# Kernel tuning notes

Hardware: AMD Instinct MI355X
Metric: run time of the kernel (lower is better)

The kernel has to match this reference:

```python
import jax, jax.numpy as jnp
import numpy as np

# TT config (matches init_kwargs)
NUM_TABLES = 4
P = (100, 100, 100)          # tt_p_shapes, prod = num_embeddings = 1e6
Q = (4, 4, 4)                # tt_q_shapes, prod = embedding_dim = 64
R = (1, 32, 32, 1)           # tt_ranks with boundary ranks
BAGS_PER_TABLE = 8192
POOL = 16                    # indices per bag


def setup_inputs() -> dict:
    key = jax.random.key(0)
    k1, k2, k3, k4 = jax.random.split(key, 4)
    nnz = NUM_TABLES * BAGS_PER_TABLE * POOL      # 524288
    B = NUM_TABLES * BAGS_PER_TABLE               # 32768 bags total
    indices = jax.random.randint(k1, (nnz,), 0, P[0] * P[1] * P[2], dtype=jnp.int64)
    offsets = (jnp.arange(B + 1, dtype=jnp.int64) * POOL)
    scale = 0.05  # small init, akin to approx-normal weight_dist
    tt_core_0 = jax.random.normal(k2, (NUM_TABLES, P[0], R[0] * Q[0] * R[1]), dtype=jnp.float32) * scale
    tt_core_1 = jax.random.normal(k3, (NUM_TABLES, P[1], R[1] * Q[1] * R[2]), dtype=jnp.float32) * scale
    tt_core_2 = jax.random.normal(k4, (NUM_TABLES, P[2], R[2] * Q[2] * R[3]), dtype=jnp.float32) * scale
    return {"indices": indices, "offsets": offsets,
            "tt_core_0": tt_core_0, "tt_core_1": tt_core_1, "tt_core_2": tt_core_2}


def reference(indices, offsets, tt_core_0, tt_core_1, tt_core_2):
    nnz = indices.shape[0]
    B = offsets.shape[0] - 1
    bags_per_table = B // NUM_TABLES

    # bag id for each nonzero (embedding-bag semantics), then table id per nonzero
    rowidx = jnp.searchsorted(offsets, jnp.arange(nnz, dtype=offsets.dtype), side='right') - 1
    tableidx = rowidx // bags_per_table

    # decompose flat row index into TT indices (C-order over p-shapes,
    # matching tt_matrix_to_full row layout)
    i0 = indices // (P[1] * P[2])
    i1 = (indices // P[2]) % P[1]
    i2 = indices % P[2]

    # gather per-lookup core slices
    c0 = tt_core_0[tableidx, i0].reshape(nnz, Q[0], R[1])          # r0 == 1
    c1 = tt_core_1[tableidx, i1].reshape(nnz, R[1], Q[1], R[2])
    c2 = tt_core_2[tableidx, i2].reshape(nnz, R[2], Q[2])          # r3 == 1

    # on-the-fly TT contraction to reconstruct embedding rows [nnz, D]
    t = jnp.einsum('nar,nrbs->nabs', c0, c1)                       # [nnz, q0, q1, r2]
    rows = jnp.einsum('nabs,nsc->nabc', t, c2).reshape(nnz, Q[0] * Q[1] * Q[2])

    # sum-pool per bag
    out = jax.ops.segment_sum(rows, rowidx, num_segments=B)        # [B, D]
    return out
```

## Files before the change

### kernel.cpp

```cpp
#include <hip/hip_runtime.h>
#include <stdint.h>

#define NT 4
#define PP 100


__device__ __forceinline__ uint32_t f2bf(float f) {
    union { float f; uint32_t u; } v; v.f = f;
    uint32_t u = v.u;
    return (u + 0x7fffu + ((u >> 16) & 1u)) >> 16;
}

__global__ __launch_bounds__(128, 3)
void tt_phase1(const float* __restrict__ c0g, const float* __restrict__ c1g,
               unsigned short* __restrict__ tT) {
    __shared__ float c1s[32 * 128];
    __shared__ float c0t[16 * 132];

    int blk = blockIdx.x;
    int tab   = blk / 700;
    int rem   = blk % 700;
    int i1    = rem / 7;
    int chunk = rem % 7;
    int i0_base = chunk * 16;
    int tid = threadIdx.x;

    const float4* c1p = (const float4*)(c1g + (size_t)(tab * PP + i1) * 4096);
    float4* c1v = (float4*)c1s;
    #pragma unroll
    for (int it = 0; it < 8; ++it) c1v[tid + 128 * it] = c1p[tid + 128 * it];

    #pragma unroll
    for (int it = 0; it < 16; ++it) {
        int f = tid + 128 * it;
        int i0l = f >> 7;
        int x   = f & 127;
        int a = x >> 5, r = x & 31;
        int i0 = i0_base + i0l; if (i0 > PP - 1) i0 = PP - 1;
        c0t[i0l * 132 + r * 4 + a] = c0g[(size_t)(tab * PP + i0) * 128 + x];
    }
    __syncthreads();

    int u  = tid >> 4;
    int sg = tid & 15;

    float acc[2][2][16];
    #pragma unroll
    for (int ii = 0; ii < 2; ++ii)
        #pragma unroll
        for (int e = 0; e < 2; ++e)
            #pragma unroll
            for (int q = 0; q < 16; ++q) acc[ii][e][q] = 0.f;

    #pragma unroll 4
    for (int r = 0; r < 32; ++r) {
        float4 av0 = *(const float4*)&c0t[(2 * u) * 132 + r * 4];
        float4 av1 = *(const float4*)&c0t[(2 * u + 1) * 132 + r * 4];
        const float* a0 = (const float*)&av0;
        const float* a1 = (const float*)&av1;
        #pragma unroll
        for (int b = 0; b < 4; ++b) {
            float2 bv = *(const float2*)&c1s[r * 128 + b * 32 + 2 * sg];
            #pragma unroll
            for (int a = 0; a < 4; ++a) {
                acc[0][0][a * 4 + b] += a0[a] * bv.x;
                acc[0][1][a * 4 + b] += a0[a] * bv.y;
                acc[1][0][a * 4 + b] += a1[a] * bv.x;
                acc[1][1][a * 4 + b] += a1[a] * bv.y;
            }
        }
    }

    #pragma unroll
    for (int ii = 0; ii < 2; ++ii) {
        int i0 = i0_base + 2 * u + ii;
        if (i0 >= PP) continue;
        size_t combo = (size_t)tab * 10000 + (size_t)i0 * 100 + (size_t)i1;
        char* base = (char*)tT + combo * 1024 + (size_t)sg * 64;
        #pragma unroll
        for (int e = 0; e < 2; ++e) {
            uint4 w0, w1;
            w0.x = f2bf(acc[ii][e][0])  | (f2bf(acc[ii][e][1])  << 16);
            w0.y = f2bf(acc[ii][e][2])  | (f2bf(acc[ii][e][3])  << 16);
            w0.z = f2bf(acc[ii][e][4])  | (f2bf(acc[ii][e][5])  << 16);
            w0.w = f2bf(acc[ii][e][6])  | (f2bf(acc[ii][e][7])  << 16);
            w1.x = f2bf(acc[ii][e][8])  | (f2bf(acc[ii][e][9])  << 16);
            w1.y = f2bf(acc[ii][e][10]) | (f2bf(acc[ii][e][11]) << 16);
            w1.z = f2bf(acc[ii][e][12]) | (f2bf(acc[ii][e][13]) << 16);
            w1.w = f2bf(acc[ii][e][14]) | (f2bf(acc[ii][e][15]) << 16);
            *(uint4*)(base + e * 32)      = w0;
            *(uint4*)(base + e * 32 + 16) = w1;
        }
    }
}

__global__ __launch_bounds__(256, 2)
void tt_phase2(const int* __restrict__ indices, const int* __restrict__ offsets,
               const unsigned short* __restrict__ tT, const float* __restrict__ c2g,
               float* __restrict__ out, int bags_per_table, int B) {
    int lane = threadIdx.x & 63;
    int wv   = threadIdx.x >> 6;
    int bag  = blockIdx.x * 4 + wv;
    if (bag >= B) return;
    int sub = lane >> 4;
    int sg  = lane & 15;
    int tab = bag / bags_per_table;
    int start = offsets[bag];

    const float* c2t = c2g + (size_t)tab * PP * 128;

    const uint4*  tp[4];
    const float4* cp[4];
    #pragma unroll
    for (int j = 0; j < 4; ++j) {
        uint32_t idx = (uint32_t)indices[start + j * 4 + sub];
        uint32_t i0 = idx / 10000u;
        uint32_t r1 = idx - i0 * 10000u;
        uint32_t i1 = r1 / 100u;
        uint32_t i2 = r1 - i1 * 100u;
        tp[j] = (const uint4*)((const char*)tT +
                 ((size_t)tab * 10000u + i0 * 100u + i1) * 1024 + (size_t)sg * 64);
        cp[j] = (const float4*)(c2t + (size_t)i2 * 128 + sg * 8);
    }

    uint4  T[4][4];
    float4 C[4][2];
    #pragma unroll
    for (int j = 0; j < 4; ++j) {
        T[j][0] = tp[j][0]; T[j][1] = tp[j][1];
        T[j][2] = tp[j][2]; T[j][3] = tp[j][3];
        C[j][0] = cp[j][0]; C[j][1] = cp[j][1];
    }

    float acc[64];
    #pragma unroll
    for (int d = 0; d < 64; ++d) acc[d] = 0.f;

    #pragma unroll
    for (int j = 0; j < 4; ++j) {
        #pragma unroll
        for (int e = 0; e < 2; ++e) {
            float4 cv = C[j][e];
            uint32_t us[8] = { T[j][2*e].x, T[j][2*e].y, T[j][2*e].z, T[j][2*e].w,
                               T[j][2*e+1].x, T[j][2*e+1].y, T[j][2*e+1].z, T[j][2*e+1].w };
            #pragma unroll
            for (int k = 0; k < 8; ++k) {
                float f0 = __uint_as_float(us[k] << 16);
                float f1 = __uint_as_float(us[k] & 0xffff0000u);
                int d0 = (2 * k) * 4, d1 = d0 + 4;
                acc[d0 + 0] += f0 * cv.x;  acc[d0 + 1] += f0 * cv.y;
                acc[d0 + 2] += f0 * cv.z;  acc[d0 + 3] += f0 * cv.w;
                acc[d1 + 0] += f1 * cv.x;  acc[d1 + 1] += f1 * cv.y;
                acc[d1 + 2] += f1 * cv.z;  acc[d1 + 3] += f1 * cv.w;
            }
        }
    }

    #pragma unroll
    for (int m = 32; m >= 1; m >>= 1) {
        bool up = (lane & m) != 0;
        #pragma unroll
        for (int j = 0; j < m; ++j) {
            float lo = acc[j], hi = acc[j + m];
            float send = up ? lo : hi;
            float recv = __shfl_xor(send, m, 64);
            acc[j] = (up ? hi : lo) + recv;
        }
    }
    out[(size_t)bag * 64 + lane] = acc[0];
}

extern "C" void kernel_launch(void* const* d_in, const int* in_sizes, int n_in,
                              void* d_out, int out_size, void* d_ws, size_t ws_size,
                              hipStream_t stream) {
    const int*   indices = (const int*)d_in[0];
    const int*   offsets = (const int*)d_in[1];
    const float* c0      = (const float*)d_in[2];
    const float* c1      = (const float*)d_in[3];
    const float* c2      = (const float*)d_in[4];
    float* out = (float*)d_out;

    int B = in_sizes[1] - 1;
    int bags_per_table = B / NT;

    unsigned short* tT = (unsigned short*)d_ws;

    tt_phase1<<<dim3(NT * PP * 7), dim3(128), 0, stream>>>(c0, c1, tT);
    tt_phase2<<<dim3((B + 3) / 4), dim3(256), 0, stream>>>(indices, offsets, tT, c2, out,
                                                           bags_per_table, B);
}
```

Baseline: 166.5 us.

## Pack c2 core to bf16 and use v_dot2_f32_bf16 in pooling kernel

```diff
diff --git a/kernel.cpp b/kernel.cpp
--- a/kernel.cpp
+++ b/kernel.cpp
@@ -3,12 +3,31 @@
 
 #define NT 4
 #define PP 100
+#define TT_BYTES (4ull * 100 * 100 * 1024)
 
 
 __device__ __forceinline__ uint32_t f2bf(float f) {
     union { float f; uint32_t u; } v; v.f = f;
     uint32_t u = v.u;
     return (u + 0x7fffu + ((u >> 16) & 1u)) >> 16;
+}
+
+__device__ __forceinline__ float dot2bf(uint32_t a, uint32_t b, float c) {
+    float d;
+    asm("v_dot2_f32_bf16 %0, %1, %2, %3" : "=v"(d) : "v"(a), "v"(b), "v"(c));
+    return d;
+}
+
+__global__ __launch_bounds__(256)
+void c2pack_kernel(const float* __restrict__ c2g, uint32_t* __restrict__ c2p) {
+    int t = blockIdx.x * 256 + threadIdx.x;
+    if (t >= NT * PP * 64) return;
+    int c = t & 3, sg = (t >> 2) & 15, rest = t >> 6;
+    int i2 = rest % PP, tab = rest / PP;
+    const float* src = c2g + (size_t)(tab * PP + i2) * 128;
+    float e = src[(2 * sg) * 4 + c];
+    float o = src[(2 * sg + 1) * 4 + c];
+    c2p[t] = f2bf(e) | (f2bf(o) << 16);
 }
 
 __global__ __launch_bounds__(128, 3)
@@ -78,25 +97,20 @@
         size_t combo = (size_t)tab * 10000 + (size_t)i0 * 100 + (size_t)i1;
         char* base = (char*)tT + combo * 1024 + (size_t)sg * 64;
         #pragma unroll
-        for (int e = 0; e < 2; ++e) {
-            uint4 w0, w1;
-            w0.x = f2bf(acc[ii][e][0])  | (f2bf(acc[ii][e][1])  << 16);
-            w0.y = f2bf(acc[ii][e][2])  | (f2bf(acc[ii][e][3])  << 16);
-            w0.z = f2bf(acc[ii][e][4])  | (f2bf(acc[ii][e][5])  << 16);
-            w0.w = f2bf(acc[ii][e][6])  | (f2bf(acc[ii][e][7])  << 16);
-            w1.x = f2bf(acc[ii][e][8])  | (f2bf(acc[ii][e][9])  << 16);
-            w1.y = f2bf(acc[ii][e][10]) | (f2bf(acc[ii][e][11]) << 16);
-            w1.z = f2bf(acc[ii][e][12]) | (f2bf(acc[ii][e][13]) << 16);
-            w1.w = f2bf(acc[ii][e][14]) | (f2bf(acc[ii][e][15]) << 16);
-            *(uint4*)(base + e * 32)      = w0;
-            *(uint4*)(base + e * 32 + 16) = w1;
-        }
-    }
-}
-
-__global__ __launch_bounds__(256, 2)
+        for (int k = 0; k < 4; ++k) {
+            uint4 w;
+            w.x = f2bf(acc[ii][0][4*k+0]) | (f2bf(acc[ii][1][4*k+0]) << 16);
+            w.y = f2bf(acc[ii][0][4*k+1]) | (f2bf(acc[ii][1][4*k+1]) << 16);
+            w.z = f2bf(acc[ii][0][4*k+2]) | (f2bf(acc[ii][1][4*k+2]) << 16);
+            w.w = f2bf(acc[ii][0][4*k+3]) | (f2bf(acc[ii][1][4*k+3]) << 16);
+            *(uint4*)(base + k * 16) = w;
+        }
+    }
+}
+
+__global__ __launch_bounds__(256, 3)
 void tt_phase2(const int* __restrict__ indices, const int* __restrict__ offsets,
-               const unsigned short* __restrict__ tT, const float* __restrict__ c2g,
+               const unsigned short* __restrict__ tT, const uint32_t* __restrict__ c2p,
                float* __restrict__ out, int bags_per_table, int B) {
     int lane = threadIdx.x & 63;
     int wv   = threadIdx.x >> 6;
@@ -107,10 +121,10 @@
     int tab = bag / bags_per_table;
     int start = offsets[bag];
 
-    const float* c2t = c2g + (size_t)tab * PP * 128;
-
-    const uint4*  tp[4];
-    const float4* cp[4];
+    const uint4* c2q = (const uint4*)c2p;
+
+    const uint4* tp[4];
+    int ci[4];
     #pragma unroll
     for (int j = 0; j < 4; ++j) {
         uint32_t idx = (uint32_t)indices[start + j * 4 + sub];
@@ -120,16 +134,16 @@
         uint32_t i2 = r1 - i1 * 100u;
         tp[j] = (const uint4*)((const char*)tT +
                  ((size_t)tab * 10000u + i0 * 100u + i1) * 1024 + (size_t)sg * 64);
-        cp[j] = (const float4*)(c2t + (size_t)i2 * 128 + sg * 8);
-    }
-
-    uint4  T[4][4];
-    float4 C[4][2];
+        ci[j] = (tab * PP + (int)i2) * 16 + sg;
+    }
+
+    uint4 T[4][4];
+    uint4 C[4];
     #pragma unroll
     for (int j = 0; j < 4; ++j) {
         T[j][0] = tp[j][0]; T[j][1] = tp[j][1];
         T[j][2] = tp[j][2]; T[j][3] = tp[j][3];
-        C[j][0] = cp[j][0]; C[j][1] = cp[j][1];
+        C[j] = c2q[ci[j]];
     }
 
     float acc[64];
@@ -138,20 +152,17 @@
 
     #pragma unroll
     for (int j = 0; j < 4; ++j) {
-        #pragma unroll
-        for (int e = 0; e < 2; ++e) {
-            float4 cv = C[j][e];
-            uint32_t us[8] = { T[j][2*e].x, T[j][2*e].y, T[j][2*e].z, T[j][2*e].w,
-                               T[j][2*e+1].x, T[j][2*e+1].y, T[j][2*e+1].z, T[j][2*e+1].w };
+        uint32_t cd[4] = { C[j].x, C[j].y, C[j].z, C[j].w };
+        #pragma unroll
+        for (int k = 0; k < 4; ++k) {
+            uint32_t td[4] = { T[j][k].x, T[j][k].y, T[j][k].z, T[j][k].w };
             #pragma unroll
-            for (int k = 0; k < 8; ++k) {
-                float f0 = __uint_as_float(us[k] << 16);
-                float f1 = __uint_as_float(us[k] & 0xffff0000u);
-                int d0 = (2 * k) * 4, d1 = d0 + 4;
-                acc[d0 + 0] += f0 * cv.x;  acc[d0 + 1] += f0 * cv.y;
-                acc[d0 + 2] += f0 * cv.z;  acc[d0 + 3] += f0 * cv.w;
-                acc[d1 + 0] += f1 * cv.x;  acc[d1 + 1] += f1 * cv.y;
-                acc[d1 + 2] += f1 * cv.z;  acc[d1 + 3] += f1 * cv.w;
+            for (int m = 0; m < 4; ++m) {
+                int d0 = (4 * k + m) * 4;
+                acc[d0 + 0] = dot2bf(td[m], cd[0], acc[d0 + 0]);
+                acc[d0 + 1] = dot2bf(td[m], cd[1], acc[d0 + 1]);
+                acc[d0 + 2] = dot2bf(td[m], cd[2], acc[d0 + 2]);
+                acc[d0 + 3] = dot2bf(td[m], cd[3], acc[d0 + 3]);
             }
         }
     }
@@ -183,9 +194,11 @@
     int B = in_sizes[1] - 1;
     int bags_per_table = B / NT;
 
-    unsigned short* tT = (unsigned short*)d_ws;
-
+    unsigned short* tT  = (unsigned short*)d_ws;
+    uint32_t*       c2p = (uint32_t*)((char*)d_ws + TT_BYTES);
+
+    c2pack_kernel<<<dim3((NT * PP * 64 + 255) / 256), dim3(256), 0, stream>>>(c2, c2p);
     tt_phase1<<<dim3(NT * PP * 7), dim3(128), 0, stream>>>(c0, c1, tT);
-    tt_phase2<<<dim3((B + 3) / 4), dim3(256), 0, stream>>>(indices, offsets, tT, c2, out,
+    tt_phase2<<<dim3((B + 3) / 4), dim3(256), 0, stream>>>(indices, offsets, tT, c2p, out,
                                                            bags_per_table, B);
 }
```

After: 155.1 us. 1.07x faster.
